# Optimization experiments

Measured on AMD Instinct MI355X. Metric: run time of the kernel, lower is better.

Reference implementation:

```python
import jax, jax.numpy as jnp
import numpy as np

B, L, E, H = 1024, 18, 300, 300
VW, VS = 100000, 2186


def setup_inputs() -> dict:
    key = jax.random.key(0)
    ks = jax.random.split(key, 16)
    word = jax.random.randint(ks[0], (B, 1), 0, VW)
    sememes = jax.random.randint(ks[1], (B, L), 0, VS)
    word_table = jax.random.normal(ks[2], (VW, E), jnp.float32) * 0.1
    sem_table = jax.random.normal(ks[3], (VS, E), jnp.float32) * 0.1
    sem_table = sem_table.at[0].set(0.0)  # padding_idx=0 -> zero row
    s = 1.0 / np.sqrt(H)

    def u(k, shape):
        return jax.random.uniform(k, shape, jnp.float32, -s, s)

    return {
        "word": word, "sememes": sememes,
        "word_table": word_table, "sem_table": sem_table,
        "Wih_f": u(ks[4], (4 * H, 2 * E)), "Whh_f": u(ks[5], (4 * H, H)),
        "bih_f": u(ks[6], (4 * H,)), "bhh_f": u(ks[7], (4 * H,)),
        "Wih_b": u(ks[8], (4 * H, 2 * E)), "Whh_b": u(ks[9], (4 * H, H)),
        "bih_b": u(ks[10], (4 * H,)), "bhh_b": u(ks[11], (4 * H,)),
        "Wa": u(ks[12], (H, 2 * H)), "ba": jnp.zeros((H,), jnp.float32),
        "Wb": u(ks[13], (E, E)), "bb": jnp.zeros((E,), jnp.float32),
    }


def _lstm(x, Wih, Whh, bih, bhh, reverse):
    # x: [B, L, 2E]; PyTorch gate order i, f, g, o
    xg = jnp.einsum('ble,ge->blg', x, Wih) + bih + bhh  # [B, L, 4H]
    Hh = Whh.shape[1]
    Bn = x.shape[0]

    def step(carry, xt):
        h, c = carry
        g = xt + h @ Whh.T
        i, f, gg, o = jnp.split(g, 4, axis=-1)
        i = jax.nn.sigmoid(i)
        f = jax.nn.sigmoid(f)
        gg = jnp.tanh(gg)
        o = jax.nn.sigmoid(o)
        c = f * c + i * gg
        h = o * jnp.tanh(c)
        return (h, c), h

    init = (jnp.zeros((Bn, Hh), x.dtype), jnp.zeros((Bn, Hh), x.dtype))
    _, hs = jax.lax.scan(step, init, jnp.swapaxes(xg, 0, 1), reverse=reverse)
    return jnp.swapaxes(hs, 0, 1)  # [B, L, H]


def reference(word, sememes, word_table, sem_table,
              Wih_f, Whh_f, bih_f, bhh_f,
              Wih_b, Whh_b, bih_b, bhh_b,
              Wa, ba, Wb, bb):
    w = word_table[word[:, 0]]      # [B, E]
    s = sem_table[sememes]          # [B, L, E]
    # AvgPool2d((18,1)) over the L=18 axis (zeros included in the mean)
    a_g = jnp.mean(s, axis=1)       # [B, E]
    v_g = jax.nn.relu(a_g @ Wb.T + bb)  # dropout is identity at inference
    # Vectorized replacement of the per-element python loop:
    # padding slot (index 0 -> zero embedding) gets cat(sem, sem) = zeros,
    # otherwise cat(word_emb, sem).
    mask = (sememes == 0)[..., None]                    # [B, L, 1]
    first = jnp.where(mask, s, w[:, None, :])           # [B, L, E]
    x = jnp.concatenate([first, s], axis=-1)            # [B, L, 2E]
    hf = _lstm(x, Wih_f, Whh_f, bih_f, bhh_f, reverse=False)
    hb = _lstm(x, Wih_b, Whh_b, bih_b, bhh_b, reverse=True)
    Vh = jnp.concatenate([hf, hb], axis=-1)             # [B, L, 2H]
    V = jax.nn.relu(jnp.einsum('blh,oh->blo', Vh, Wa) + ba)
    return V, v_g
```

## Files before the change

kernel.cpp:

```cpp
#include <hip/hip_runtime.h>
#include <hip/hip_cooperative_groups.h>
#include <cstddef>
#include <cstdint>
#include <math.h>

namespace cg = cooperative_groups;

#define B_   1024
#define L_   18
#define E_   300
#define H_   300
#define M_   (B_*L_)
#define G4_  (4*H_)
#define K2E_ (2*E_)

#define NPAD 2432
#define PSTR 2432
#define M2P  2304

#define OFF_P1   ((size_t)0)
#define OFF_P2   (OFF_P1 + (size_t)1024*PSTR)
#define OFF_HCAT (OFF_P2 + (size_t)M2P*PSTR)
#define OFF_AG   (OFF_HCAT + (size_t)M_*608/2)
#define OFF_WBT  (OFF_AG  + (size_t)B_*E_)
#define OFF_WFF  (OFF_WBT + 90000)
#define OFF_WFB  (OFF_WFF + 194560)
#define OFF_WAT  (OFF_WFB + 194560)
#define OFF_WCP  (OFF_WAT + 92416)
#define OFF_HP   (OFF_WCP + 778240)
#define OFF_C    (OFF_HP + 655360)

#define HPSTR 327680

#define VOFF ((size_t)M_*H_)

typedef short bf16x8 __attribute__((ext_vector_type(8)));
typedef float f32x4  __attribute__((ext_vector_type(4)));

__device__ __forceinline__ short f2bf(float f) {
    union { float f; uint32_t u; } c; c.f = f;
    uint32_t u = c.u + 0x7fffu + ((c.u >> 16) & 1u);
    return (short)(u >> 16);
}

__global__ void k_prep(const float* __restrict__ Wb, float* __restrict__ WbT)
{
    int idx = blockIdx.x * 256 + threadIdx.x;
    if (idx < 90000) {
        int o = idx % 300;
        int k = idx / 300;
        WbT[idx] = Wb[o * 300 + k];
    }
}

__global__ __launch_bounds__(256) void k_prep_wcp(const float* __restrict__ Wih_f,
                                                  const float* __restrict__ Wih_b,
                                                  short* __restrict__ WcatP)
{
    int idx = blockIdx.x * 256 + threadIdx.x;
    if (idx >= 2 * NPAD * 320) return;
    int p = idx / (NPAD * 320);
    int rem = idx - p * (NPAD * 320);
    int n = rem / 320;
    int kp = rem - n * 320;
    int fwd = (n < 1216);
    int nn = fwd ? n : n - 1216;
    float v = 0.f;
    if (kp < 300 && nn < G4_) {
        int u = nn >> 2, g = nn & 3;
        const float* W = fwd ? Wih_f : Wih_b;
        v = W[(size_t)(g * 300 + u) * K2E_ + (p ? 300 + kp : kp)];
    }
    WcatP[idx] = f2bf(v);
}

__global__ __launch_bounds__(256) void k_prep_whh(const float* __restrict__ Whh_f,
                                                  const float* __restrict__ Whh_b,
                                                  short* __restrict__ WFf,
                                                  short* __restrict__ WFb)
{
    int idx = blockIdx.x * 256 + threadIdx.x;
    if (idx >= 389120) return;
    int d = blockIdx.y;
    int chunk = idx >> 9;
    int rem   = idx & 511;
    int lane  = rem >> 3;
    int j     = rem & 7;
    int nt = chunk / 10, kt = chunk - nt * 10;
    int n = nt * 16 + (lane & 15);
    int k = kt * 32 + (lane >> 4) * 8 + j;
    float v = 0.f;
    if (n < G4_ && k < H_) {
        int u = n >> 2, g = n & 3;
        const float* W = d ? Whh_b : Whh_f;
        v = W[(size_t)(g * 300 + u) * H_ + k];
    }
    (d ? WFb : WFf)[idx] = f2bf(v);
}

__global__ __launch_bounds__(256) void k_prep_wa(const float* __restrict__ Wa,
                                                 short* __restrict__ WAT)
{
    int idx = blockIdx.x * 256 + threadIdx.x;
    if (idx >= 184832) return;
    int chunk = idx >> 9;
    int rem   = idx & 511;
    int lane  = rem >> 3;
    int j     = rem & 7;
    int nt = chunk / 19, kt = chunk - nt * 19;
    int o  = nt * 16 + (lane & 15);
    int kp = kt * 32 + (lane >> 4) * 8 + j;
    float v = 0.f;
    if (o < H_) {
        int k = -1;
        if (kp < 300)                   k = kp;
        else if (kp >= 304 && kp < 604) k = kp - 4;
        if (k >= 0) v = Wa[(size_t)o * K2E_ + k];
    }
    WAT[idx] = f2bf(v);
}

__global__ __launch_bounds__(256) void k_ag(const int* __restrict__ sem,
                                            const float* __restrict__ sem_table,
                                            float* __restrict__ ag)
{
    int b = blockIdx.x;
    __shared__ int sm[L_];
    if (threadIdx.x < L_) sm[threadIdx.x] = sem[b * L_ + threadIdx.x];
    __syncthreads();
    for (int e = threadIdx.x; e < E_; e += 256) {
        float s = 0.f;
        #pragma unroll
        for (int l = 0; l < L_; ++l) s += sem_table[sm[l] * E_ + e];
        ag[(size_t)b * E_ + e] = s * (1.0f / (float)L_);
    }
}

__global__ __launch_bounds__(256) void k_vg(const float* __restrict__ ag,
                                            const float* __restrict__ WbT,
                                            const float* __restrict__ bbv,
                                            float* __restrict__ out)
{
    int b0 = blockIdx.x * 16;
    __shared__ __align__(16) float ag_s[16 * E_];
    for (int idx = threadIdx.x; idx < 16 * E_; idx += 256)
        ag_s[idx] = ag[(size_t)b0 * E_ + idx];
    __syncthreads();
    for (int o = threadIdx.x; o < E_; o += 256) {
        float acc[16];
        #pragma unroll
        for (int i = 0; i < 16; ++i) acc[i] = 0.f;
        for (int k = 0; k < E_; ++k) {
            float w = WbT[k * E_ + o];
            #pragma unroll
            for (int i = 0; i < 16; ++i)
                acc[i] = fmaf(w, ag_s[i * E_ + k], acc[i]);
        }
        float bias = bbv[o];
        #pragma unroll
        for (int i = 0; i < 16; ++i) {
            float v = acc[i] + bias;
            out[VOFF + (size_t)(b0 + i) * E_ + o] = v > 0.f ? v : 0.f;
        }
    }
}

#define LDT 40

__global__ __launch_bounds__(256) void k_p(const int* __restrict__ word,
                                           const float* __restrict__ word_table,
                                           const float* __restrict__ sem_table,
                                           const short* __restrict__ WcatP,
                                           const float* __restrict__ bih_f,
                                           const float* __restrict__ bhh_f,
                                           const float* __restrict__ bih_b,
                                           const float* __restrict__ bhh_b,
                                           float* __restrict__ P1,
                                           float* __restrict__ P2)
{
    __shared__ __align__(16) short As[128 * LDT];
    __shared__ __align__(16) short Bs[128 * LDT];
    __shared__ const float* rowp[128];

    const int mb = blockIdx.x;
    const int p  = (mb >= 8);
    const int m0 = (p ? mb - 8 : mb) * 128;
    const int n0 = blockIdx.y * 128;
    const int tid = threadIdx.x;

    if (tid < 128) {
        int m = m0 + tid;
        rowp[tid] = p ? (m < 2186 ? sem_table + (size_t)m * E_ : (const float*)0)
                      : word_table + (size_t)word[m] * E_;
    }
    __syncthreads();

    f32x4 acc[4][4];
    #pragma unroll
    for (int i = 0; i < 4; ++i)
        #pragma unroll
        for (int j = 0; j < 4; ++j)
            acc[i][j] = (f32x4){0.f, 0.f, 0.f, 0.f};

    const int wv   = tid >> 6;
    const int lane = tid & 63;
    const int wm   = (wv >> 1) * 64;
    const int wn   = (wv & 1) * 64;
    const int lm   = lane & 15;
    const int quad = lane >> 4;

    const int r  = tid >> 1;
    const int kh = (tid & 1) * 16;
    const float* rp = rowp[r];
    const short* bsrc = WcatP + (size_t)p * (NPAD * 320) + (size_t)(n0 + r) * 320;

    for (int k0 = 0; k0 < 320; k0 += 32) {
        {
            const int kbase = k0 + kh;
            #pragma unroll
            for (int q = 0; q < 4; ++q) {
                int k = kbase + q * 4;
                float4 v = (k < E_ && rp) ? *(const float4*)&rp[k]
                                          : make_float4(0.f, 0.f, 0.f, 0.f);
                short4 s4;
                s4.x = f2bf(v.x); s4.y = f2bf(v.y);
                s4.z = f2bf(v.z); s4.w = f2bf(v.w);
                *(short4*)&As[r * LDT + kh + q * 4] = s4;
            }
        }
        {
            const short* src = bsrc + k0 + kh;
            *(int4*)&Bs[r * LDT + kh + 0] = *(const int4*)&src[0];
            *(int4*)&Bs[r * LDT + kh + 8] = *(const int4*)&src[8];
        }
        __syncthreads();

        bf16x8 af[4], bfr[4];
        #pragma unroll
        for (int i = 0; i < 4; ++i)
            af[i] = *(const bf16x8*)&As[(wm + 16 * i + lm) * LDT + quad * 8];
        #pragma unroll
        for (int j = 0; j < 4; ++j)
            bfr[j] = *(const bf16x8*)&Bs[(wn + 16 * j + lm) * LDT + quad * 8];
        #pragma unroll
        for (int i = 0; i < 4; ++i)
            #pragma unroll
            for (int j = 0; j < 4; ++j)
                acc[i][j] = __builtin_amdgcn_mfma_f32_16x16x32_bf16(
                    af[i], bfr[j], acc[i][j], 0, 0, 0);
        __syncthreads();
    }

    float* dst = p ? P2 : P1;
    #pragma unroll
    for (int j = 0; j < 4; ++j) {
        int n = n0 + wn + 16 * j + lm;
        float bias = 0.f;
        if (p) {
            int fwd = (n < 1216);
            int cc = fwd ? n : n - 1216;
            if (cc < G4_) {
                int u = cc >> 2, g = cc & 3;
                bias = fwd ? (bih_f[g * 300 + u] + bhh_f[g * 300 + u])
                           : (bih_b[g * 300 + u] + bhh_b[g * 300 + u]);
            }
        }
        #pragma unroll
        for (int i = 0; i < 4; ++i) {
            int mb2 = m0 + wm + 16 * i + quad * 4;
            #pragma unroll
            for (int reg = 0; reg < 4; ++reg)
                dst[(size_t)(mb2 + reg) * PSTR + n] = acc[i][j][reg] + bias;
        }
    }
}

__global__ __launch_bounds__(256, 2) void k_rec2(const float* __restrict__ P1,
                                                 const float* __restrict__ P2,
                                                 const int* __restrict__ sem,
                                                 const short* __restrict__ WFf,
                                                 const short* __restrict__ WFb,
                                                 short* __restrict__ hp,
                                                 short* __restrict__ hcat)
{
    cg::grid_group gg = cg::this_grid();

    const int d  = blockIdx.z;
    const short* WF = d ? WFb : WFf;
    short* hc = hcat + (d ? 304 : 0);
    const int rt0 = blockIdx.x * 8;
    const int nb  = blockIdx.y;
    const int tid  = threadIdx.x;
    const int lane = tid & 63;
    const int wv   = tid >> 6;
    const int quad = lane >> 4;

    __shared__ __align__(16) float Cs[128][68];

    bf16x8 bfr[10];
    {
        const short* wp = WF + ((size_t)(nb * 4 + wv) * 10) * 512 + lane * 8;
        #pragma unroll
        for (int kt = 0; kt < 10; ++kt)
            bfr[kt] = *(const bf16x8*)(wp + kt * 512);
    }

    const int m  = tid >> 1;
    const int q  = tid & 1;
    const int b  = rt0 * 16 + m;
    const int u0 = nb * 16 + 8 * q;
    const bool a0 = (u0 < H_);
    const bool a1 = (u0 + 4 < H_);
    const size_t pcol = (size_t)d * 1216 + 4 * u0;
    const float* p1r = P1 + (size_t)b * PSTR + pcol;
    float c8[8] = {0.f,0.f,0.f,0.f,0.f,0.f,0.f,0.f};

    size_t hofs;
    {
        int rt = b >> 4, ktu = u0 >> 5;
        int fl = (b & 15) | (((u0 >> 3) & 3) << 4);
        hofs = ((size_t)(rt * 10 + ktu) * 512) + (size_t)fl * 8 + (u0 & 7);
    }

    for (int s = 0; s < L_; ++s) {
        const int t = d ? (L_ - 1 - s) : s;
        const short* hin = hp + (size_t)(d * 2 + ((s + 1) & 1)) * HPSTR;
        short*      hout = hp + (size_t)(d * 2 + (s & 1)) * HPSTR;

        float4 xv[8];
        {
            const int svt = sem[b * L_ + t];
            const float* p2r = P2 + (size_t)svt * PSTR + pcol;
            #pragma unroll
            for (int i = 0; i < 8; ++i) xv[i] = *(const float4*)&p2r[4 * i];
            if (svt != 0) {
                #pragma unroll
                for (int i = 0; i < 8; ++i) {
                    float4 a = *(const float4*)&p1r[4 * i];
                    xv[i].x += a.x; xv[i].y += a.y; xv[i].z += a.z; xv[i].w += a.w;
                }
            }
        }

        f32x4 acc[8];
        #pragma unroll
        for (int mt = 0; mt < 8; ++mt) acc[mt] = (f32x4){0.f, 0.f, 0.f, 0.f};
        if (s > 0) {
            #pragma unroll
            for (int kt = 0; kt < 10; ++kt) {
                #pragma unroll
                for (int mt = 0; mt < 8; ++mt) {
                    bf16x8 af = *(const bf16x8*)&hin[((size_t)(rt0 + mt) * 10 + kt) * 512 + lane * 8];
                    acc[mt] = __builtin_amdgcn_mfma_f32_16x16x32_bf16(af, bfr[kt], acc[mt], 0, 0, 0);
                }
            }
        }

        #pragma unroll
        for (int mt = 0; mt < 8; ++mt)
            #pragma unroll
            for (int r = 0; r < 4; ++r)
                Cs[mt * 16 + quad * 4 + r][wv * 16 + (lane & 15)] = acc[mt][r];
        __syncthreads();

        {
            short hn[8];
            #pragma unroll
            for (int i = 0; i < 8; ++i) {
                float4 gv = *(const float4*)&Cs[m][32 * q + 4 * i];
                float gi = xv[i].x + gv.x;
                float gf = xv[i].y + gv.y;
                float gg2 = xv[i].z + gv.z;
                float go = xv[i].w + gv.w;
                float iv = 1.f / (1.f + __expf(-gi));
                float fv = 1.f / (1.f + __expf(-gf));
                float tg = 1.f - 2.f / (__expf(2.f * gg2) + 1.f);
                float ov = 1.f / (1.f + __expf(-go));
                float cc = fmaf(fv, c8[i], iv * tg);
                c8[i] = cc;
                float th = 1.f - 2.f / (__expf(2.f * cc) + 1.f);
                hn[i] = f2bf(ov * th);
            }
            if (a0) {
                short4 h4 = {hn[0], hn[1], hn[2], hn[3]};
                *(short4*)&hout[hofs] = h4;
                *(short4*)&hc[((size_t)b * L_ + t) * 608 + u0] = h4;
            }
            if (a1) {
                short4 h4 = {hn[4], hn[5], hn[6], hn[7]};
                *(short4*)&hout[hofs + 4] = h4;
                *(short4*)&hc[((size_t)b * L_ + t) * 608 + u0 + 4] = h4;
            }
        }

        __threadfence();
        gg.sync();
    }
}

__global__ __launch_bounds__(256) void k_step2(const float* __restrict__ P1,
                                               const float* __restrict__ P2,
                                               const int* __restrict__ sem,
                                               const short* __restrict__ WFf,
                                               const short* __restrict__ WFb,
                                               short* __restrict__ hp,
                                               float* __restrict__ cbuf,
                                               short* __restrict__ hcat,
                                               int s)
{
    const int d  = blockIdx.z;
    const short* WF = d ? WFb : WFf;
    const int t = d ? (L_ - 1 - s) : s;
    const short* hin = hp + (size_t)(d * 2 + ((s + 1) & 1)) * HPSTR;
    short*      hout = hp + (size_t)(d * 2 + (s & 1)) * HPSTR;
    short* hc = hcat + (d ? 304 : 0);
    float* cp = cbuf + (size_t)d * (1024 * 304);

    const int m0 = blockIdx.x * 64;
    const int rt0 = blockIdx.x * 4;
    const int nb = blockIdx.y;
    const int tid  = threadIdx.x;
    const int lane = tid & 63;
    const int wv   = tid >> 6;
    const int quad = lane >> 4;

    __shared__ __align__(16) float Cs[64][68];

    f32x4 acc[4];
    #pragma unroll
    for (int mt = 0; mt < 4; ++mt) acc[mt] = (f32x4){0.f, 0.f, 0.f, 0.f};

    if (s > 0) {
        const short* wp = WF + ((size_t)(nb * 4 + wv) * 10) * 512 + lane * 8;
        #pragma unroll
        for (int kt = 0; kt < 10; ++kt) {
            bf16x8 bf = *(const bf16x8*)(wp + kt * 512);
            #pragma unroll
            for (int mt = 0; mt < 4; ++mt) {
                bf16x8 af = *(const bf16x8*)&hin[((size_t)(rt0 + mt) * 10 + kt) * 512 + lane * 8];
                acc[mt] = __builtin_amdgcn_mfma_f32_16x16x32_bf16(af, bf, acc[mt], 0, 0, 0);
            }
        }
    }

    #pragma unroll
    for (int mt = 0; mt < 4; ++mt)
        #pragma unroll
        for (int r = 0; r < 4; ++r)
            Cs[mt * 16 + quad * 4 + r][wv * 16 + (lane & 15)] = acc[mt][r];
    __syncthreads();

    const int m = tid >> 2;
    const int q = tid & 3;
    const int b = m0 + m;
    const int u0 = nb * 16 + 4 * q;
    if (u0 < H_) {
        const int svt = sem[b * L_ + t];
        const size_t pcol = (size_t)d * 1216 + 4 * u0;
        const float* p2r = P2 + (size_t)svt * PSTR + pcol;
        const float* p1r = P1 + (size_t)b * PSTR + pcol;
        float4 xv[4];
        #pragma unroll
        for (int i = 0; i < 4; ++i) xv[i] = *(const float4*)&p2r[4 * i];
        if (svt != 0) {
            #pragma unroll
            for (int i = 0; i < 4; ++i) {
                float4 a = *(const float4*)&p1r[4 * i];
                xv[i].x += a.x; xv[i].y += a.y; xv[i].z += a.z; xv[i].w += a.w;
            }
        }
        float4 cpv = (s > 0) ? *(const float4*)&cp[(size_t)b * 304 + u0]
                             : make_float4(0.f, 0.f, 0.f, 0.f);
        float cold[4] = {cpv.x, cpv.y, cpv.z, cpv.w};
        float cnew[4];
        short hn[4];
        #pragma unroll
        for (int i = 0; i < 4; ++i) {
            float4 gv = *(const float4*)&Cs[m][16 * q + 4 * i];
            float gi = xv[i].x + gv.x;
            float gf = xv[i].y + gv.y;
            float gg = xv[i].z + gv.z;
            float go = xv[i].w + gv.w;
            float iv = 1.f / (1.f + __expf(-gi));
            float fv = 1.f / (1.f + __expf(-gf));
            float tg = 1.f - 2.f / (__expf(2.f * gg) + 1.f);
            float ov = 1.f / (1.f + __expf(-go));
            float cc = fmaf(fv, cold[i], iv * tg);
            cnew[i] = cc;
            float th = 1.f - 2.f / (__expf(2.f * cc) + 1.f);
            hn[i] = f2bf(ov * th);
        }
        *(float4*)&cp[(size_t)b * 304 + u0] = make_float4(cnew[0], cnew[1], cnew[2], cnew[3]);
        short4 h4 = {hn[0], hn[1], hn[2], hn[3]};
        {
            int rt = b >> 4, ktu = u0 >> 5;
            int fl = (b & 15) | (((u0 >> 3) & 3) << 4);
            *(short4*)&hout[((size_t)(rt * 10 + ktu) * 512) + (size_t)fl * 8 + (u0 & 7)] = h4;
        }
        *(short4*)&hc[((size_t)b * L_ + t) * 608 + u0] = h4;
    }
}

__global__ __launch_bounds__(256) void k_out(const short* __restrict__ hcat,
                                             const short* __restrict__ WAT,
                                             const float* __restrict__ ba,
                                             float* __restrict__ out)
{
    const int m0 = blockIdx.x * 64;
    const int tid = threadIdx.x;
    const int lane = tid & 63;
    const int wv = tid >> 6;
    const int lm = lane & 15;
    const int quad = lane >> 4;

    __shared__ __align__(16) short A_s[64][616];

    for (int idx = tid; idx < 4864; idx += 256) {
        int r = idx / 76, c8 = idx - r * 76;
        *(int4*)&A_s[r][c8 * 8] = *(const int4*)&hcat[(size_t)(m0 + r) * 608 + c8 * 8];
    }
    __syncthreads();

    f32x4 acc[4][5];
    #pragma unroll
    for (int mt = 0; mt < 4; ++mt)
        #pragma unroll
        for (int q = 0; q < 5; ++q)
            acc[mt][q] = (f32x4){0.f, 0.f, 0.f, 0.f};

    for (int kt = 0; kt < 19; ++kt) {
        bf16x8 af[4];
        #pragma unroll
        for (int mt = 0; mt < 4; ++mt)
            af[mt] = *(const bf16x8*)&A_s[mt * 16 + lm][kt * 32 + quad * 8];
        #pragma unroll
        for (int q = 0; q < 5; ++q) {
            int nt = wv + 4 * q;
            if (nt < 19) {
                bf16x8 bf = *(const bf16x8*)&WAT[((size_t)(nt * 19 + kt) * 64 + lane) * 8];
                #pragma unroll
                for (int mt = 0; mt < 4; ++mt)
                    acc[mt][q] = __builtin_amdgcn_mfma_f32_16x16x32_bf16(
                        af[mt], bf, acc[mt][q], 0, 0, 0);
            }
        }
    }

    #pragma unroll
    for (int q = 0; q < 5; ++q) {
        int nt = wv + 4 * q;
        if (nt < 19) {
            int o = nt * 16 + lm;
            if (o < H_) {
                float bias = ba[o];
                #pragma unroll
                for (int mt = 0; mt < 4; ++mt) {
                    #pragma unroll
                    for (int r = 0; r < 4; ++r) {
                        int m = m0 + mt * 16 + quad * 4 + r;
                        float v = acc[mt][q][r] + bias;
                        out[(size_t)m * H_ + o] = v > 0.f ? v : 0.f;
                    }
                }
            }
        }
    }
}

extern "C" void kernel_launch(void* const* d_in, const int* in_sizes, int n_in,
                              void* d_out, int out_size, void* d_ws, size_t ws_size,
                              hipStream_t stream) {
    const int*   word       = (const int*)  d_in[0];
    const int*   sem        = (const int*)  d_in[1];
    const float* word_table = (const float*)d_in[2];
    const float* sem_table  = (const float*)d_in[3];
    const float* Wih_f      = (const float*)d_in[4];
    const float* Whh_f      = (const float*)d_in[5];
    const float* bih_f      = (const float*)d_in[6];
    const float* bhh_f      = (const float*)d_in[7];
    const float* Wih_b      = (const float*)d_in[8];
    const float* Whh_b      = (const float*)d_in[9];
    const float* bih_b      = (const float*)d_in[10];
    const float* bhh_b      = (const float*)d_in[11];
    const float* Wa         = (const float*)d_in[12];
    const float* ba         = (const float*)d_in[13];
    const float* Wb         = (const float*)d_in[14];
    const float* bbv        = (const float*)d_in[15];

    float* out = (float*)d_out;
    float* ws  = (float*)d_ws;

    float* P1    = ws + OFF_P1;
    float* P2    = ws + OFF_P2;
    short* hcat  = (short*)(ws + OFF_HCAT);
    float* ag    = ws + OFF_AG;
    float* WbT   = ws + OFF_WBT;
    short* WFf   = (short*)(ws + OFF_WFF);
    short* WFb   = (short*)(ws + OFF_WFB);
    short* WAT   = (short*)(ws + OFF_WAT);
    short* WcatP = (short*)(ws + OFF_WCP);
    short* hp    = (short*)(ws + OFF_HP);
    float* cbuf  = ws + OFF_C;

    k_prep<<<dim3(352), dim3(256), 0, stream>>>(Wb, WbT);
    k_prep_wcp<<<dim3((2 * NPAD * 320 + 255) / 256), dim3(256), 0, stream>>>(
        Wih_f, Wih_b, WcatP);
    k_prep_whh<<<dim3(1520, 2), dim3(256), 0, stream>>>(Whh_f, Whh_b, WFf, WFb);
    k_prep_wa<<<dim3(722), dim3(256), 0, stream>>>(Wa, WAT);

    k_ag<<<dim3(B_), dim3(256), 0, stream>>>(sem, sem_table, ag);
    k_vg<<<dim3(B_ / 16), dim3(256), 0, stream>>>(ag, WbT, bbv, out);

    k_p<<<dim3(26, 19), dim3(256), 0, stream>>>(
        word, word_table, sem_table, WcatP,
        bih_f, bhh_f, bih_b, bhh_b, P1, P2);

    int useCoop = 0;
    {
        int dev = 0, coopAttr = 0, numCU = 0, maxBlk = 0;
        (void)hipGetDevice(&dev);
        (void)hipDeviceGetAttribute(&coopAttr, hipDeviceAttributeCooperativeLaunch, dev);
        (void)hipDeviceGetAttribute(&numCU, hipDeviceAttributeMultiprocessorCount, dev);
        (void)hipOccupancyMaxActiveBlocksPerMultiprocessor(&maxBlk, k_rec2, 256, 0);
        if (coopAttr && (long)maxBlk * (long)numCU >= 304) useCoop = 1;
    }
    if (useCoop) {
        void* args[] = {(void*)&P1, (void*)&P2, (void*)&sem,
                        (void*)&WFf, (void*)&WFb, (void*)&hp, (void*)&hcat};
        hipError_t e = hipLaunchCooperativeKernel((const void*)k_rec2,
                                                  dim3(8, 19, 2), dim3(256),
                                                  args, 0, stream);
        if (e != hipSuccess) useCoop = 0;
    }
    if (!useCoop) {
        for (int s = 0; s < L_; ++s) {
            k_step2<<<dim3(16, 19, 2), dim3(256), 0, stream>>>(
                P1, P2, sem, WFf, WFb, hp, cbuf, hcat, s);
        }
    }

    k_out<<<dim3(M_ / 64), dim3(256), 0, stream>>>(hcat, WAT, ba, out);
}
```

Baseline: 531.6 us.

## Replace grid-synchronized LSTM recurrence with batch-partitioned per-block recurrence kernel

Drops the cooperative kernel (and its per-step fallback) that split the gate dimension across blocks and needed a grid-wide barrier every timestep. Each block now owns 32 batch rows and all gate columns, so it can run all 18 steps on its own. The hidden state lives in shared memory and the cell state in an LDS array. Recurrent weights are streamed from global/L2 every step through a triple-buffered register prefetch. This removes the grid syncs and the global h round-trips, but launches only 64 blocks and rereads the full Whh per block per step, which puts heavy pressure on L2 bandwidth.

Measured after the change: 819.8 us. 1.54x slower.

```diff
diff --git a/kernel.cpp b/kernel.cpp
--- a/kernel.cpp
+++ b/kernel.cpp
@@ -1,10 +1,7 @@
 #include <hip/hip_runtime.h>
-#include <hip/hip_cooperative_groups.h>
 #include <cstddef>
 #include <cstdint>
 #include <math.h>
-
-namespace cg = cooperative_groups;
 
 #define B_   1024
 #define L_   18
@@ -27,10 +24,6 @@
 #define OFF_WFB  (OFF_WFF + 194560)
 #define OFF_WAT  (OFF_WFB + 194560)
 #define OFF_WCP  (OFF_WAT + 92416)
-#define OFF_HP   (OFF_WCP + 778240)
-#define OFF_C    (OFF_HP + 655360)
-
-#define HPSTR 327680
 
 #define VOFF ((size_t)M_*H_)
 
@@ -275,229 +268,114 @@
     }
 }
 
-__global__ __launch_bounds__(256, 2) void k_rec2(const float* __restrict__ P1,
-                                                 const float* __restrict__ P2,
-                                                 const int* __restrict__ sem,
-                                                 const short* __restrict__ WFf,
-                                                 const short* __restrict__ WFb,
-                                                 short* __restrict__ hp,
-                                                 short* __restrict__ hcat)
-{
-    cg::grid_group gg = cg::this_grid();
-
-    const int d  = blockIdx.z;
+#define NT_BODY(I, BCUR, BNXT, PF)                                            \
+  {                                                                           \
+    if (PF) {                                                                 \
+      const short* wn = wfp + (size_t)((I) + 2) * 5120;                       \
+      _Pragma("unroll")                                                       \
+      for (int kt = 0; kt < 10; ++kt)                                         \
+        BNXT[kt] = *(const bf16x8*)(wn + kt * 512);                           \
+    }                                                                         \
+    float4 xv = *(const float4*)(p2r + 16 * (I));                             \
+    if (svt != 0) {                                                           \
+      float4 a4 = *(const float4*)(p1r + 16 * (I));                           \
+      xv.x += a4.x; xv.y += a4.y; xv.z += a4.z; xv.w += a4.w;                 \
+    }                                                                         \
+    f32x4 acc = (f32x4){0.f, 0.f, 0.f, 0.f};                                  \
+    if (s > 0) {                                                              \
+      _Pragma("unroll")                                                       \
+      for (int kt = 0; kt < 10; ++kt)                                         \
+        acc = __builtin_amdgcn_mfma_f32_16x16x32_bf16(BCUR[kt], af[kt],       \
+                                                      acc, 0, 0, 0);          \
+    }                                                                         \
+    float gi  = xv.x + acc[0];                                                \
+    float gf  = xv.y + acc[1];                                                \
+    float gg2 = xv.z + acc[2];                                                \
+    float go  = xv.w + acc[3];                                                \
+    float iv = 1.f / (1.f + __expf(-gi));                                     \
+    float fv = 1.f / (1.f + __expf(-gf));                                     \
+    float tg = 1.f - 2.f / (__expf(2.f * gg2) + 1.f);                         \
+    float ov = 1.f / (1.f + __expf(-go));                                     \
+    float cc = fmaf(fv, cst[cslot + (I)], iv * tg);                           \
+    cst[cslot + (I)] = cc;                                                    \
+    float th = 1.f - 2.f / (__expf(2.f * cc) + 1.f);                          \
+    short hv = f2bf(ov * th);                                                 \
+    int u = unt0 + 4 * (I);                                                   \
+    hbuf[(mt * 10 + (u >> 5)) * 512 + ((lr | (((u >> 3) & 3) << 4)) << 3)     \
+         + (u & 7)] = hv;                                                     \
+    hcrow[u] = hv;                                                            \
+  }
+
+__global__ __launch_bounds__(512) void k_rec3(const float* __restrict__ P1,
+                                              const float* __restrict__ P2,
+                                              const int* __restrict__ sem,
+                                              const short* __restrict__ WFf,
+                                              const short* __restrict__ WFb,
+                                              short* __restrict__ hcat)
+{
+    const int d = blockIdx.y;
     const short* WF = d ? WFb : WFf;
     short* hc = hcat + (d ? 304 : 0);
-    const int rt0 = blockIdx.x * 8;
-    const int nb  = blockIdx.y;
+
+    const int b0   = blockIdx.x * 32;
     const int tid  = threadIdx.x;
     const int lane = tid & 63;
     const int wv   = tid >> 6;
-    const int quad = lane >> 4;
-
-    __shared__ __align__(16) float Cs[128][68];
-
-    bf16x8 bfr[10];
-    {
-        const short* wp = WF + ((size_t)(nb * 4 + wv) * 10) * 512 + lane * 8;
-        #pragma unroll
-        for (int kt = 0; kt < 10; ++kt)
-            bfr[kt] = *(const bf16x8*)(wp + kt * 512);
-    }
-
-    const int m  = tid >> 1;
-    const int q  = tid & 1;
-    const int b  = rt0 * 16 + m;
-    const int u0 = nb * 16 + 8 * q;
-    const bool a0 = (u0 < H_);
-    const bool a1 = (u0 + 4 < H_);
-    const size_t pcol = (size_t)d * 1216 + 4 * u0;
-    const float* p1r = P1 + (size_t)b * PSTR + pcol;
-    float c8[8] = {0.f,0.f,0.f,0.f,0.f,0.f,0.f,0.f};
-
-    size_t hofs;
-    {
-        int rt = b >> 4, ktu = u0 >> 5;
-        int fl = (b & 15) | (((u0 >> 3) & 3) << 4);
-        hofs = ((size_t)(rt * 10 + ktu) * 512) + (size_t)fl * 8 + (u0 & 7);
-    }
-
+    const int nq   = wv & 3;
+    const int mt   = wv >> 2;
+    const int lr   = lane & 15;
+    const int lu   = lane >> 4;
+    const int b    = b0 + mt * 16 + lr;
+    const int unt0 = nq * 76 + lu;
+    const int cslot = tid * 19;
+
+    __shared__ __align__(16) short hbuf[2 * 10 * 512];
+    __shared__ __align__(16) float cst[512 * 19];
+
+    for (int idx = tid; idx < 1280; idx += 512)
+        ((int4*)hbuf)[idx] = make_int4(0, 0, 0, 0);
+    for (int idx = tid; idx < 2432; idx += 512)
+        ((float4*)cst)[idx] = make_float4(0.f, 0.f, 0.f, 0.f);
+    __syncthreads();
+
+    const size_t pbase = (size_t)d * 1216 + (size_t)nq * 304 + (size_t)lu * 4;
+    const float* p1r = P1 + (size_t)b * PSTR + pbase;
+    const float* p2b = P2 + pbase;
+    const short* wfp = WF + (size_t)(nq * 19) * 5120 + (size_t)lane * 8;
+
+    #pragma unroll 1
     for (int s = 0; s < L_; ++s) {
         const int t = d ? (L_ - 1 - s) : s;
-        const short* hin = hp + (size_t)(d * 2 + ((s + 1) & 1)) * HPSTR;
-        short*      hout = hp + (size_t)(d * 2 + (s & 1)) * HPSTR;
-
-        float4 xv[8];
-        {
-            const int svt = sem[b * L_ + t];
-            const float* p2r = P2 + (size_t)svt * PSTR + pcol;
+        const int svt = sem[b * L_ + t];
+        const float* p2r = p2b + (size_t)svt * PSTR;
+        short* hcrow = hc + ((size_t)b * L_ + t) * 608;
+
+        bf16x8 bA[10], bB[10], bC[10];
+        #pragma unroll
+        for (int kt = 0; kt < 10; ++kt)
+            bA[kt] = *(const bf16x8*)(wfp + kt * 512);
+        #pragma unroll
+        for (int kt = 0; kt < 10; ++kt)
+            bB[kt] = *(const bf16x8*)(wfp + 5120 + kt * 512);
+
+        bf16x8 af[10];
+        if (s > 0) {
+            const short* hb = hbuf + mt * 5120 + lane * 8;
             #pragma unroll
-            for (int i = 0; i < 8; ++i) xv[i] = *(const float4*)&p2r[4 * i];
-            if (svt != 0) {
-                #pragma unroll
-                for (int i = 0; i < 8; ++i) {
-                    float4 a = *(const float4*)&p1r[4 * i];
-                    xv[i].x += a.x; xv[i].y += a.y; xv[i].z += a.z; xv[i].w += a.w;
-                }
-            }
-        }
-
-        f32x4 acc[8];
-        #pragma unroll
-        for (int mt = 0; mt < 8; ++mt) acc[mt] = (f32x4){0.f, 0.f, 0.f, 0.f};
-        if (s > 0) {
-            #pragma unroll
-            for (int kt = 0; kt < 10; ++kt) {
-                #pragma unroll
-                for (int mt = 0; mt < 8; ++mt) {
-                    bf16x8 af = *(const bf16x8*)&hin[((size_t)(rt0 + mt) * 10 + kt) * 512 + lane * 8];
-                    acc[mt] = __builtin_amdgcn_mfma_f32_16x16x32_bf16(af, bfr[kt], acc[mt], 0, 0, 0);
-                }
-            }
-        }
-
-        #pragma unroll
-        for (int mt = 0; mt < 8; ++mt)
-            #pragma unroll
-            for (int r = 0; r < 4; ++r)
-                Cs[mt * 16 + quad * 4 + r][wv * 16 + (lane & 15)] = acc[mt][r];
+            for (int kt = 0; kt < 10; ++kt)
+                af[kt] = *(const bf16x8*)(hb + kt * 512);
+        }
         __syncthreads();
 
-        {
-            short hn[8];
-            #pragma unroll
-            for (int i = 0; i < 8; ++i) {
-                float4 gv = *(const float4*)&Cs[m][32 * q + 4 * i];
-                float gi = xv[i].x + gv.x;
-                float gf = xv[i].y + gv.y;
-                float gg2 = xv[i].z + gv.z;
-                float go = xv[i].w + gv.w;
-                float iv = 1.f / (1.f + __expf(-gi));
-                float fv = 1.f / (1.f + __expf(-gf));
-                float tg = 1.f - 2.f / (__expf(2.f * gg2) + 1.f);
-                float ov = 1.f / (1.f + __expf(-go));
-                float cc = fmaf(fv, c8[i], iv * tg);
-                c8[i] = cc;
-                float th = 1.f - 2.f / (__expf(2.f * cc) + 1.f);
-                hn[i] = f2bf(ov * th);
-            }
-            if (a0) {
-                short4 h4 = {hn[0], hn[1], hn[2], hn[3]};
-                *(short4*)&hout[hofs] = h4;
-                *(short4*)&hc[((size_t)b * L_ + t) * 608 + u0] = h4;
-            }
-            if (a1) {
-                short4 h4 = {hn[4], hn[5], hn[6], hn[7]};
-                *(short4*)&hout[hofs + 4] = h4;
-                *(short4*)&hc[((size_t)b * L_ + t) * 608 + u0 + 4] = h4;
-            }
-        }
-
-        __threadfence();
-        gg.sync();
-    }
-}
-
-__global__ __launch_bounds__(256) void k_step2(const float* __restrict__ P1,
-                                               const float* __restrict__ P2,
-                                               const int* __restrict__ sem,
-                                               const short* __restrict__ WFf,
-                                               const short* __restrict__ WFb,
-                                               short* __restrict__ hp,
-                                               float* __restrict__ cbuf,
-                                               short* __restrict__ hcat,
-                                               int s)
-{
-    const int d  = blockIdx.z;
-    const short* WF = d ? WFb : WFf;
-    const int t = d ? (L_ - 1 - s) : s;
-    const short* hin = hp + (size_t)(d * 2 + ((s + 1) & 1)) * HPSTR;
-    short*      hout = hp + (size_t)(d * 2 + (s & 1)) * HPSTR;
-    short* hc = hcat + (d ? 304 : 0);
-    float* cp = cbuf + (size_t)d * (1024 * 304);
-
-    const int m0 = blockIdx.x * 64;
-    const int rt0 = blockIdx.x * 4;
-    const int nb = blockIdx.y;
-    const int tid  = threadIdx.x;
-    const int lane = tid & 63;
-    const int wv   = tid >> 6;
-    const int quad = lane >> 4;
-
-    __shared__ __align__(16) float Cs[64][68];
-
-    f32x4 acc[4];
-    #pragma unroll
-    for (int mt = 0; mt < 4; ++mt) acc[mt] = (f32x4){0.f, 0.f, 0.f, 0.f};
-
-    if (s > 0) {
-        const short* wp = WF + ((size_t)(nb * 4 + wv) * 10) * 512 + lane * 8;
-        #pragma unroll
-        for (int kt = 0; kt < 10; ++kt) {
-            bf16x8 bf = *(const bf16x8*)(wp + kt * 512);
-            #pragma unroll
-            for (int mt = 0; mt < 4; ++mt) {
-                bf16x8 af = *(const bf16x8*)&hin[((size_t)(rt0 + mt) * 10 + kt) * 512 + lane * 8];
-                acc[mt] = __builtin_amdgcn_mfma_f32_16x16x32_bf16(af, bf, acc[mt], 0, 0, 0);
-            }
-        }
-    }
-
-    #pragma unroll
-    for (int mt = 0; mt < 4; ++mt)
-        #pragma unroll
-        for (int r = 0; r < 4; ++r)
-            Cs[mt * 16 + quad * 4 + r][wv * 16 + (lane & 15)] = acc[mt][r];
-    __syncthreads();
-
-    const int m = tid >> 2;
-    const int q = tid & 3;
-    const int b = m0 + m;
-    const int u0 = nb * 16 + 4 * q;
-    if (u0 < H_) {
-        const int svt = sem[b * L_ + t];
-        const size_t pcol = (size_t)d * 1216 + 4 * u0;
-        const float* p2r = P2 + (size_t)svt * PSTR + pcol;
-        const float* p1r = P1 + (size_t)b * PSTR + pcol;
-        float4 xv[4];
-        #pragma unroll
-        for (int i = 0; i < 4; ++i) xv[i] = *(const float4*)&p2r[4 * i];
-        if (svt != 0) {
-            #pragma unroll
-            for (int i = 0; i < 4; ++i) {
-                float4 a = *(const float4*)&p1r[4 * i];
-                xv[i].x += a.x; xv[i].y += a.y; xv[i].z += a.z; xv[i].w += a.w;
-            }
-        }
-        float4 cpv = (s > 0) ? *(const float4*)&cp[(size_t)b * 304 + u0]
-                             : make_float4(0.f, 0.f, 0.f, 0.f);
-        float cold[4] = {cpv.x, cpv.y, cpv.z, cpv.w};
-        float cnew[4];
-        short hn[4];
-        #pragma unroll
-        for (int i = 0; i < 4; ++i) {
-            float4 gv = *(const float4*)&Cs[m][16 * q + 4 * i];
-            float gi = xv[i].x + gv.x;
-            float gf = xv[i].y + gv.y;
-            float gg = xv[i].z + gv.z;
-            float go = xv[i].w + gv.w;
-            float iv = 1.f / (1.f + __expf(-gi));
-            float fv = 1.f / (1.f + __expf(-gf));
-            float tg = 1.f - 2.f / (__expf(2.f * gg) + 1.f);
-            float ov = 1.f / (1.f + __expf(-go));
-            float cc = fmaf(fv, cold[i], iv * tg);
-            cnew[i] = cc;
-            float th = 1.f - 2.f / (__expf(2.f * cc) + 1.f);
-            hn[i] = f2bf(ov * th);
-        }
-        *(float4*)&cp[(size_t)b * 304 + u0] = make_float4(cnew[0], cnew[1], cnew[2], cnew[3]);
-        short4 h4 = {hn[0], hn[1], hn[2], hn[3]};
-        {
-            int rt = b >> 4, ktu = u0 >> 5;
-            int fl = (b & 15) | (((u0 >> 3) & 3) << 4);
-            *(short4*)&hout[((size_t)(rt * 10 + ktu) * 512) + (size_t)fl * 8 + (u0 & 7)] = h4;
-        }
-        *(short4*)&hc[((size_t)b * L_ + t) * 608 + u0] = h4;
+        #pragma unroll 1
+        for (int i = 0; i < 18; i += 3) {
+            NT_BODY(i,     bA, bC, 1)
+            NT_BODY(i + 1, bB, bA, 1)
+            NT_BODY(i + 2, bC, bB, (i < 15))
+        }
+        NT_BODY(18, bA, bC, 0)
+
+        __syncthreads();
     }
 }
 
@@ -599,8 +477,6 @@
     short* WFb   = (short*)(ws + OFF_WFB);
     short* WAT   = (short*)(ws + OFF_WAT);
     short* WcatP = (short*)(ws + OFF_WCP);
-    short* hp    = (short*)(ws + OFF_HP);
-    float* cbuf  = ws + OFF_C;
 
     k_prep<<<dim3(352), dim3(256), 0, stream>>>(Wb, WbT);
     k_prep_wcp<<<dim3((2 * NPAD * 320 + 255) / 256), dim3(256), 0, stream>>>(
@@ -615,29 +491,7 @@
         word, word_table, sem_table, WcatP,
         bih_f, bhh_f, bih_b, bhh_b, P1, P2);
 
-    int useCoop = 0;
-    {
-        int dev = 0, coopAttr = 0, numCU = 0, maxBlk = 0;
-        (void)hipGetDevice(&dev);
-        (void)hipDeviceGetAttribute(&coopAttr, hipDeviceAttributeCooperativeLaunch, dev);
-        (void)hipDeviceGetAttribute(&numCU, hipDeviceAttributeMultiprocessorCount, dev);
-        (void)hipOccupancyMaxActiveBlocksPerMultiprocessor(&maxBlk, k_rec2, 256, 0);
-        if (coopAttr && (long)maxBlk * (long)numCU >= 304) useCoop = 1;
-    }
-    if (useCoop) {
-        void* args[] = {(void*)&P1, (void*)&P2, (void*)&sem,
-                        (void*)&WFf, (void*)&WFb, (void*)&hp, (void*)&hcat};
-        hipError_t e = hipLaunchCooperativeKernel((const void*)k_rec2,
-                                                  dim3(8, 19, 2), dim3(256),
-                                                  args, 0, stream);
-        if (e != hipSuccess) useCoop = 0;
-    }
-    if (!useCoop) {
-        for (int s = 0; s < L_; ++s) {
-            k_step2<<<dim3(16, 19, 2), dim3(256), 0, stream>>>(
-                P1, P2, sem, WFf, WFb, hp, cbuf, hcat, s);
-        }
-    }
+    k_rec3<<<dim3(32, 2), dim3(512), 0, stream>>>(P1, P2, sem, WFf, WFb, hcat);
 
     k_out<<<dim3(M_ / 64), dim3(256), 0, stream>>>(hcat, WAT, ba, out);
 }
```
